# Kernel optimization log

Measured on AMD Instinct MI355X. Metric: run time of the kernel, lower is better.

Reference implementation:

```python
import jax, jax.numpy as jnp
import numpy as np

B_SZ, SEQ, D_MODEL, N_STATE = 4, 2048, 768, 16


def setup_inputs() -> dict:
    key = jax.random.key(0)
    ks = jax.random.split(key, 8)
    s = 1.0 / np.sqrt(D_MODEL)
    x = jax.random.normal(ks[0], (B_SZ, SEQ, D_MODEL), dtype=jnp.float32)
    W1 = jax.random.uniform(ks[1], (D_MODEL, D_MODEL), jnp.float32, -s, s)
    b1 = jax.random.uniform(ks[2], (D_MODEL,), jnp.float32, -s, s)
    W2 = jax.random.uniform(ks[3], (D_MODEL, N_STATE), jnp.float32, -s, s)
    b2 = jax.random.uniform(ks[4], (N_STATE,), jnp.float32, -s, s)
    W3 = jax.random.uniform(ks[5], (D_MODEL, N_STATE), jnp.float32, -s, s)
    b3 = jax.random.uniform(ks[6], (N_STATE,), jnp.float32, -s, s)
    # A: xavier_uniform over (d_model, state_size)
    a_bound = np.sqrt(6.0 / (D_MODEL + N_STATE))
    A = jax.random.uniform(ks[7], (D_MODEL, N_STATE), jnp.float32, -a_bound, a_bound)
    return {"x": x, "W1": W1, "b1": b1, "W2": W2, "b2": b2, "W3": W3, "b3": b3, "A": A}


def reference(x, W1, b1, W2, b2, W3, b3, A):
    # Input-dependent projections
    Bm = x @ W2 + b2                     # [b, l, n]
    Cm = x @ W3 + b3                     # [b, l, n]
    delta = jax.nn.softplus(x @ W1 + b1)  # [b, l, d]
    # Discretization (S6)
    dB = delta[..., None] * Bm[:, :, None, :]                 # [b, l, d, n]
    dA = jnp.exp(jnp.einsum('bld,dn->bldn', delta, A))        # [b, l, d, n]
    # Source initializes h to zeros, so the dA*h term vanishes (no recurrence).
    h0 = jnp.zeros_like(dB)
    h = dA * h0 + x[..., None] * dB                            # [b, l, d, n]
    y = jnp.einsum('bln,bldn->bld', Cm, h)                     # [b, l, d]
    return y
```

## Files before the change

### kernel.cpp

```cpp
#include <hip/hip_runtime.h>
#include <hip/hip_bf16.h>
#include <math.h>


#define M_ROWS 8192
#define DM 768
#define NS 16
#define NT 12

typedef short bf16x8 __attribute__((ext_vector_type(8)));
typedef unsigned short u16x8 __attribute__((ext_vector_type(8)));
typedef float f32x4 __attribute__((ext_vector_type(4)));

__device__ __forceinline__ unsigned short f2bf(float f) {
    union { float f; unsigned u; } v; v.f = f;
    unsigned r = v.u + 0x7FFF + ((v.u >> 16) & 1);
    return (unsigned short)(r >> 16);
}
__device__ __forceinline__ unsigned short cvtbf(float f) {
    __hip_bfloat16 h = __float2bfloat16(f);
    return *reinterpret_cast<unsigned short*>(&h);
}
__device__ __forceinline__ void async16(const void* g, void* l) {
    __builtin_amdgcn_global_load_lds(
        (const __attribute__((address_space(1))) void*)g,
        (__attribute__((address_space(3))) void*)l,
        16, 0, 0);
}
__device__ __forceinline__ float softplus_fast(float v) {
    return fmaxf(v, 0.f) + __logf(1.f + __expf(-fabsf(v)));
}

__global__ __launch_bounds__(256) void prep_kernel(
    const float* __restrict__ W1,
    const float* __restrict__ W2,
    const float* __restrict__ W3,
    unsigned short* __restrict__ w1t,
    unsigned short* __restrict__ w23t)
{
    __shared__ float tile[32][33];
    const int bid = blockIdx.x;
    const int tid = threadIdx.x;
    if (bid < 32) {
        const int n = bid, i = n >> 1;
        const float* src = (n & 1) ? W3 : W2;
        #pragma unroll
        for (int e = 0; e < 3; ++e) {
            int k = e * 256 + tid;
            w23t[n * DM + k] = f2bf(src[k * NS + i]);
        }
    } else {
        const int b2i = bid - 32;
        const int n0 = (b2i % 24) * 32, k0 = (b2i / 24) * 32;
        const int tx = tid & 31, ty = tid >> 5;
        #pragma unroll
        for (int i = 0; i < 4; ++i) {
            int k = ty + i * 8;
            tile[k][tx] = W1[(k0 + k) * DM + n0 + tx];
        }
        __syncthreads();
        #pragma unroll
        for (int i = 0; i < 4; ++i) {
            int n = ty + i * 8;
            w1t[(n0 + n) * DM + k0 + tx] = f2bf(tile[tx][n]);
        }
    }
}

__global__ __launch_bounds__(256) void gemm_fused_kernel(
    const float* __restrict__ x,
    const unsigned short* __restrict__ w1t,
    const unsigned short* __restrict__ w23t,
    const float* __restrict__ b1,
    const float* __restrict__ b2, const float* __restrict__ b3,
    float* __restrict__ y)
{
    __shared__ unsigned short Al[2][128 * 64];
    __shared__ unsigned short Bl[2][64 * 64];
    __shared__ float spart[2][128];
    const int b = blockIdx.x;
    const int c = b & 7, j = b >> 3;
    const int m0 = (c * 8 + j / 12) * 128;
    const int n0 = (j % 12) * 64;
    const int tid  = threadIdx.x;
    const int lane = tid & 63;
    const int wave = tid >> 6;
    const int wm = wave >> 1, wn = wave & 1;
    const int l15 = lane & 15, quad = lane >> 4;

    f32x4 acc[4][2];
    f32x4 accP[4];
    #pragma unroll
    for (int i = 0; i < 4; ++i) {
        accP[i] = (f32x4){0.f, 0.f, 0.f, 0.f};
        #pragma unroll
        for (int jj = 0; jj < 2; ++jj)
            acc[i][jj] = (f32x4){0.f, 0.f, 0.f, 0.f};
    }

    float4 va[8];
    bf16x8 vw[2][2];

#define LOAD_A(T) do {                                                     \
        const int k0_ = (T) * 64;                                          \
        _Pragma("unroll")                                                  \
        for (int i_ = 0; i_ < 4; ++i_) {                                   \
            int ch_ = tid + i_ * 256;                                      \
            int r_ = ch_ >> 3, jg_ = (ch_ & 7) ^ (r_ & 7);                 \
            const float4* s_ = (const float4*)(x + (m0 + r_) * DM + k0_ + jg_ * 8); \
            va[2 * i_]     = s_[0];                                        \
            va[2 * i_ + 1] = s_[1];                                        \
        }                                                                  \
    } while (0)

#define LOAD_W(P, T) do {                                                  \
        const int k0_ = (T) * 64;                                          \
        const int rw_ = wn * 16 + l15;                                     \
        _Pragma("unroll")                                                  \
        for (int kk_ = 0; kk_ < 2; ++kk_)                                  \
            vw[P][kk_] = *(const bf16x8*)(w23t + rw_ * DM + k0_ + (kk_ * 4 + quad) * 8); \
    } while (0)

#define STAGE_B(P, T) do {                                                 \
        const int k0_ = (T) * 64;                                          \
        _Pragma("unroll")                                                  \
        for (int i_ = 0; i_ < 2; ++i_) {                                   \
            int ch_ = tid + i_ * 256;                                      \
            int r_ = ch_ >> 3, jg_ = (ch_ & 7) ^ (r_ & 7);                 \
            async16(w1t + (n0 + r_) * DM + k0_ + jg_ * 8, &Bl[P][ch_ * 8]); \
        }                                                                  \
    } while (0)

#define CVT_WRITE_A(P) do {                                                \
        _Pragma("unroll")                                                  \
        for (int i_ = 0; i_ < 4; ++i_) {                                   \
            int ch_ = tid + i_ * 256;                                      \
            float4 a_ = va[2 * i_], b_ = va[2 * i_ + 1];                   \
            u16x8 o_;                                                      \
            o_[0] = cvtbf(a_.x); o_[1] = cvtbf(a_.y);                      \
            o_[2] = cvtbf(a_.z); o_[3] = cvtbf(a_.w);                      \
            o_[4] = cvtbf(b_.x); o_[5] = cvtbf(b_.y);                      \
            o_[6] = cvtbf(b_.z); o_[7] = cvtbf(b_.w);                      \
            *(u16x8*)(&Al[P][ch_ * 8]) = o_;                               \
        }                                                                  \
    } while (0)

    LOAD_A(0);
    LOAD_W(0, 0);
    STAGE_B(0, 0);
    CVT_WRITE_A(0);
    LOAD_A(1);
    LOAD_W(1, 1);
    __syncthreads();
    STAGE_B(1, 1);

    #pragma unroll
    for (int t = 0; t < NT; ++t) {
        const int cur = t & 1;
        #pragma unroll
        for (int kk = 0; kk < 2; ++kk) {
            bf16x8 bfr[2];
            #pragma unroll
            for (int jj = 0; jj < 2; ++jj) {
                int rb = wn * 32 + jj * 16 + l15;
                int jb = (kk * 4 + quad) ^ (rb & 7);
                bfr[jj] = *(const bf16x8*)(&Bl[cur][rb * 64 + jb * 8]);
            }
            bf16x8 wfr = vw[cur][kk];
            #pragma unroll
            for (int i = 0; i < 4; ++i) {
                int rr = wm * 64 + i * 16 + l15;
                int ja = (kk * 4 + quad) ^ (rr & 7);
                bf16x8 af = *(const bf16x8*)(&Al[cur][rr * 64 + ja * 8]);
                #pragma unroll
                for (int jj = 0; jj < 2; ++jj)
                    acc[i][jj] = __builtin_amdgcn_mfma_f32_16x16x32_bf16(
                        af, bfr[jj], acc[i][jj], 0, 0, 0);
                accP[i] = __builtin_amdgcn_mfma_f32_16x16x32_bf16(
                    af, wfr, accP[i], 0, 0, 0);
            }
        }
        if (t + 1 < NT) {
            CVT_WRITE_A(cur ^ 1);
            __syncthreads();
            if (t + 2 < NT) {
                LOAD_A(t + 2);
                LOAD_W(cur, t + 2);
                STAGE_B(cur, t + 2);
            }
        }
    }

    {
        const int p = wn * 8 + (l15 >> 1);
        const float bB = b2[p], bC = b3[p];
        #pragma unroll
        for (int i = 0; i < 4; ++i) {
            float sacc[4];
            #pragma unroll
            for (int r = 0; r < 4; ++r) {
                float v = accP[i][r];
                float pv = __shfl_xor(v, 1, 64);
                sacc[r] = (l15 & 1) ? (pv + bB) * (v + bC)
                                    : (v + bB) * (pv + bC);
                sacc[r] += __shfl_xor(sacc[r], 1, 64);
                sacc[r] += __shfl_xor(sacc[r], 2, 64);
                sacc[r] += __shfl_xor(sacc[r], 4, 64);
                sacc[r] += __shfl_xor(sacc[r], 8, 64);
            }
            if (l15 == 0) {
                #pragma unroll
                for (int r = 0; r < 4; ++r)
                    spart[wn][wm * 64 + i * 16 + quad * 4 + r] = 0.5f * sacc[r];
            }
        }
    }
    __syncthreads();

    #pragma unroll
    for (int i = 0; i < 4; ++i) {
        const int rl = wm * 64 + i * 16 + quad * 4;
        const int rowbase = m0 + rl;
        float sv4[4];
        #pragma unroll
        for (int r = 0; r < 4; ++r)
            sv4[r] = spart[0][rl + r] + spart[1][rl + r];
        #pragma unroll
        for (int jj = 0; jj < 2; ++jj) {
            int gcol = n0 + wn * 32 + jj * 16 + l15;
            float bias = b1[gcol];
            #pragma unroll
            for (int r = 0; r < 4; ++r) {
                int grow = rowbase + r;
                float v = acc[i][jj][r] + bias;
                float sp = softplus_fast(v);
                float xv = x[grow * DM + gcol];
                y[grow * DM + gcol] = xv * sp * sv4[r];
            }
        }
    }
#undef LOAD_A
#undef LOAD_W
#undef STAGE_B
#undef CVT_WRITE_A
}

extern "C" void kernel_launch(void* const* d_in, const int* in_sizes, int n_in,
                              void* d_out, int out_size, void* d_ws, size_t ws_size,
                              hipStream_t stream) {
    const float* x  = (const float*)d_in[0];
    const float* W1 = (const float*)d_in[1];
    const float* b1 = (const float*)d_in[2];
    const float* W2 = (const float*)d_in[3];
    const float* b2 = (const float*)d_in[4];
    const float* W3 = (const float*)d_in[5];
    const float* b3 = (const float*)d_in[6];
    float* y = (float*)d_out;

    unsigned short* w1t  = (unsigned short*)d_ws;
    unsigned short* w23t = (unsigned short*)((char*)d_ws + 1179648);

    prep_kernel<<<608, 256, 0, stream>>>(W1, W2, W3, w1t, w23t);
    gemm_fused_kernel<<<768, 256, 0, stream>>>(x, w1t, w23t, b1, b2, b3, y);
}
```

Before: 120.8 us.

## Double-buffer A register prefetch with manual waitcnt and sched barriers

Adds a second register buffer for the fp32 x tile so the global load for tile t+2 is issued before the MFMA loop of tile t rather than after the barrier. The __syncthreads calls become explicit s_waitcnt vmcnt(8) plus s_barrier, with sched_barrier fences to pin instruction order, so outstanding A loads need not drain at each barrier. It also adds a launch-bounds occupancy hint of 3. The extra 32 registers and the hint could cause spills, and the hand-counted vmcnt values must match the exact number of loads issued.

```diff
diff --git a/kernel.cpp b/kernel.cpp
--- a/kernel.cpp
+++ b/kernel.cpp
@@ -30,6 +30,8 @@
 __device__ __forceinline__ float softplus_fast(float v) {
     return fmaxf(v, 0.f) + __logf(1.f + __expf(-fabsf(v)));
 }
+
+#define FENCE() __builtin_amdgcn_sched_barrier(0)
 
 __global__ __launch_bounds__(256) void prep_kernel(
     const float* __restrict__ W1,
@@ -67,7 +69,7 @@
     }
 }
 
-__global__ __launch_bounds__(256) void gemm_fused_kernel(
+__global__ __launch_bounds__(256, 3) void gemm_fused_kernel(
     const float* __restrict__ x,
     const unsigned short* __restrict__ w1t,
     const unsigned short* __restrict__ w23t,
@@ -98,18 +100,18 @@
             acc[i][jj] = (f32x4){0.f, 0.f, 0.f, 0.f};
     }
 
-    float4 va[8];
+    float4 va[2][8];
     bf16x8 vw[2][2];
 
-#define LOAD_A(T) do {                                                     \
+#define LOAD_A(P, T) do {                                                  \
         const int k0_ = (T) * 64;                                          \
         _Pragma("unroll")                                                  \
         for (int i_ = 0; i_ < 4; ++i_) {                                   \
             int ch_ = tid + i_ * 256;                                      \
             int r_ = ch_ >> 3, jg_ = (ch_ & 7) ^ (r_ & 7);                 \
             const float4* s_ = (const float4*)(x + (m0 + r_) * DM + k0_ + jg_ * 8); \
-            va[2 * i_]     = s_[0];                                        \
-            va[2 * i_ + 1] = s_[1];                                        \
+            va[P][2 * i_]     = s_[0];                                     \
+            va[P][2 * i_ + 1] = s_[1];                                     \
         }                                                                  \
     } while (0)
 
@@ -135,7 +137,7 @@
         _Pragma("unroll")                                                  \
         for (int i_ = 0; i_ < 4; ++i_) {                                   \
             int ch_ = tid + i_ * 256;                                      \
-            float4 a_ = va[2 * i_], b_ = va[2 * i_ + 1];                   \
+            float4 a_ = va[P][2 * i_], b_ = va[P][2 * i_ + 1];             \
             u16x8 o_;                                                      \
             o_[0] = cvtbf(a_.x); o_[1] = cvtbf(a_.y);                      \
             o_[2] = cvtbf(a_.z); o_[3] = cvtbf(a_.w);                      \
@@ -145,18 +147,27 @@
         }                                                                  \
     } while (0)
 
-    LOAD_A(0);
+    LOAD_A(0, 0);
     LOAD_W(0, 0);
     STAGE_B(0, 0);
+    FENCE();
+    LOAD_A(1, 1);
+    FENCE();
     CVT_WRITE_A(0);
-    LOAD_A(1);
+    FENCE();
+    asm volatile("s_waitcnt vmcnt(8) lgkmcnt(0)" ::: "memory");
+    FENCE();
+    __builtin_amdgcn_s_barrier();
+    FENCE();
     LOAD_W(1, 1);
-    __syncthreads();
     STAGE_B(1, 1);
+    FENCE();
 
     #pragma unroll
     for (int t = 0; t < NT; ++t) {
         const int cur = t & 1;
+        if (t + 2 < NT) { LOAD_A(cur, t + 2); }
+        FENCE();
         #pragma unroll
         for (int kk = 0; kk < 2; ++kk) {
             bf16x8 bfr[2];
@@ -180,14 +191,20 @@
                     af, wfr, accP[i], 0, 0, 0);
             }
         }
+        FENCE();
         if (t + 1 < NT) {
             CVT_WRITE_A(cur ^ 1);
-            __syncthreads();
+            FENCE();
             if (t + 2 < NT) {
-                LOAD_A(t + 2);
-                LOAD_W(cur, t + 2);
-                STAGE_B(cur, t + 2);
-            }
+                asm volatile("s_waitcnt vmcnt(8) lgkmcnt(0)" ::: "memory");
+            } else {
+                asm volatile("s_waitcnt vmcnt(0) lgkmcnt(0)" ::: "memory");
+            }
+            FENCE();
+            __builtin_amdgcn_s_barrier();
+            FENCE();
+            if (t + 2 < NT) { LOAD_W(cur, t + 2); STAGE_B(cur, t + 2); }
+            FENCE();
         }
     }
 
```

New measurement: 120.3 us. About the same (-0.4%).
